# Kernel tuning notes

Hardware: AMD Instinct MI355X
Metric: run time of the kernel (lower is better)

Reference implementation:

```python
import jax, jax.numpy as jnp
import numpy as np

D_MODEL = 1024
NHEAD = 16
HEAD_DIM = D_MODEL // NHEAD  # 64
THETA = 10000.0


def apply_rope(t):
    # t: [B, H, S, D]. Interleaved-pair RoPE (lucidrains rotary-embedding-torch
    # rotate_queries_or_keys), positions = arange(S), theta = 10000.
    B, H, S, D = t.shape
    inv_freq = 1.0 / (THETA ** (jnp.arange(0, D, 2, dtype=jnp.float32) / D))  # [D/2]
    ang = jnp.arange(S, dtype=jnp.float32)[:, None] * inv_freq               # [S, D/2]
    cos = jnp.cos(ang).astype(t.dtype)
    sin = jnp.sin(ang).astype(t.dtype)
    tp = t.reshape(B, H, S, D // 2, 2)
    x1, x2 = tp[..., 0], tp[..., 1]
    rot = jnp.stack([x1 * cos - x2 * sin, x1 * sin + x2 * cos], axis=-1)
    return rot.reshape(B, H, S, D)


def setup_inputs() -> dict:
    key = jax.random.key(0)
    k0, k1, k2, k3, k4 = jax.random.split(key, 5)
    B, Sx, Sc = 2, 2048, 2048
    sc = 0.02  # weight init scale
    return {
        "x": jax.random.normal(k0, (B, Sx, D_MODEL), jnp.float32),
        "context": jax.random.normal(k1, (B, Sc, D_MODEL), jnp.float32),
        "Wq": jax.random.normal(k2, (D_MODEL, D_MODEL), jnp.float32) * sc,
        "Wv": jax.random.normal(k3, (D_MODEL, D_MODEL), jnp.float32) * sc,
        "Wo": jax.random.normal(k4, (D_MODEL, D_MODEL), jnp.float32) * sc,
        "bo": jnp.zeros((D_MODEL,), jnp.float32),
        "x_pos": jnp.arange(B * Sx, dtype=jnp.int64).reshape(B, Sx) % Sx,
        "context_pos": jnp.arange(B * Sc, dtype=jnp.int64).reshape(B, Sc) % Sc,
    }


def reference(x, context, Wq, Wv, Wo, bo, x_pos, context_pos):
    # x_pos/context_pos are unused when both streams use the internal
    # RotaryEmbedding (is_imu1=is_imu2=True), matching the original forward.
    B, Sx, _ = x.shape
    Sc = context.shape[1]
    q = (x @ Wq.T).reshape(B, Sx, NHEAD, HEAD_DIM).transpose(0, 2, 1, 3)
    # NOTE: original code uses projq (not projk) for keys — replicated here.
    k = (context @ Wq.T).reshape(B, Sc, NHEAD, HEAD_DIM).transpose(0, 2, 1, 3)
    v = (context @ Wv.T).reshape(B, Sc, NHEAD, HEAD_DIM).transpose(0, 2, 1, 3)
    q = apply_rope(q)
    k = apply_rope(k)
    scale = 1.0 / jnp.sqrt(jnp.asarray(HEAD_DIM, q.dtype))
    attn = jax.nn.softmax(jnp.einsum("bhqd,bhkd->bhqk", q, k) * scale, axis=-1)
    out = jnp.einsum("bhqk,bhkd->bhqd", attn, v)            # [B,H,Sx,hd]
    out = out.transpose(0, 2, 1, 3).reshape(B, Sx, D_MODEL)  # [B,Sx,d_model]
    return out @ Wo.T + bo
```

## Files before the change

kernel.cpp:

```cpp
#include <hip/hip_runtime.h>
#include <cmath>


typedef __bf16 bf16x8 __attribute__((ext_vector_type(8)));
typedef __bf16 bf16x4 __attribute__((ext_vector_type(4)));
typedef float f32x4 __attribute__((ext_vector_type(4)));

#define MFMA(A, B, C) __builtin_amdgcn_mfma_f32_16x16x32_bf16(A, B, C, 0, 0, 0)
#define GLL16(g, l)                                                        \
  __builtin_amdgcn_global_load_lds(                                        \
      (const __attribute__((address_space(1))) unsigned int*)(g),          \
      (__attribute__((address_space(3))) unsigned int*)(l), 16, 0, 0)

__global__ __launch_bounds__(256) void cvt_all_kernel(
    const float* __restrict__ x, const float* __restrict__ ctx,
    const float* __restrict__ Wq, const float* __restrict__ Wv,
    const float* __restrict__ Wo, __bf16* __restrict__ xb, __bf16* __restrict__ cb,
    __bf16* __restrict__ Wqb, __bf16* __restrict__ Wvb, __bf16* __restrict__ Wob) {
  int base = blockIdx.x * 512 + threadIdx.x;
  const float* src;
  __bf16* dst;
  int off;
  if (base < 1048576) { src = x; dst = xb; off = 0; }
  else if (base < 2097152) { src = ctx; dst = cb; off = 1048576; }
  else if (base < 2359296) { src = Wq; dst = Wqb; off = 2097152; }
  else if (base < 2621440) { src = Wv; dst = Wvb; off = 2359296; }
  else { src = Wo; dst = Wob; off = 2621440; }
#pragma unroll
  for (int jj = 0; jj < 2; jj++) {
    int j = base - off + jj * 256;
    float4 f = ((const float4*)src)[j];
    bf16x4 o;
    o[0] = (__bf16)f.x; o[1] = (__bf16)f.y; o[2] = (__bf16)f.z; o[3] = (__bf16)f.w;
    ((bf16x4*)dst)[j] = o;
  }
}

__global__ __launch_bounds__(256) void gemm_proj(const __bf16* __restrict__ A0,
                                                 const __bf16* __restrict__ W0,
                                                 void* __restrict__ outQ,
                                                 void* __restrict__ outK,
                                                 void* __restrict__ outV) {
  const int tid = threadIdx.x;
  const int wave = tid >> 6, lane = tid & 63, quad = lane >> 4, l15 = lane & 15;
  const int mw = wave >> 1, nw = wave & 1;

  const int id = blockIdx.x;
  int m0, n0;
  const __bf16* A;
  const __bf16* W;
  bool vmode;
  if (id < 512) {
    const int xcd = id & 7, j = id >> 3;
    m0 = (xcd * 8 + (j & 7)) * 128;
    n0 = (j >> 3) * 128;
    A = A0;
    W = W0;
    vmode = false;
  } else {
    const int vid = id - 512;
    const int xcd = vid & 7, j = vid >> 3;
    m0 = (xcd * 4 + (j & 3)) * 128;
    n0 = (j >> 2) * 128;
    A = A0 + (size_t)4096 * 1024;
    W = W0 + (size_t)1024 * 1024;
    vmode = true;
  }

  __shared__ __attribute__((aligned(16))) __bf16 As[3][4096];
  __shared__ __attribute__((aligned(16))) __bf16 Ws[3][4096];

  int goff[2];
#pragma unroll
  for (int jj = 0; jj < 2; jj++) {
    const int s = jj * 256 + tid;
    const int row = s >> 2;
    const int kcg = (s & 3) ^ ((row >> 1) & 3);
    goff[jj] = row * 1024 + kcg * 8;
  }
  const __bf16* Ag = A + (size_t)m0 * 1024;
  const __bf16* Wg = W + (size_t)n0 * 1024;
  const int ldsoff0 = wave * 512;
  const int ldsoff1 = 2048 + wave * 512;

  const int sw = (l15 >> 1) & 3;
  int afoff[4], wfoff[4];
#pragma unroll
  for (int t = 0; t < 4; t++) {
    afoff[t] = (mw * 64 + t * 16 + l15) * 32 + (quad ^ sw) * 8;
    wfoff[t] = (nw * 64 + t * 16 + l15) * 32 + (quad ^ sw) * 8;
  }

  f32x4 acc[4][4] = {};

  auto stage = [&](int buf, int k0) {
    GLL16(Ag + goff[0] + k0, &As[buf][ldsoff0]);
    GLL16(Ag + goff[1] + k0, &As[buf][ldsoff1]);
    GLL16(Wg + goff[0] + k0, &Ws[buf][ldsoff0]);
    GLL16(Wg + goff[1] + k0, &Ws[buf][ldsoff1]);
  };
  auto compute = [&](int buf) {
    bf16x8 af[4], wf[4];
#pragma unroll
    for (int t = 0; t < 4; t++) af[t] = *(const bf16x8*)&As[buf][afoff[t]];
#pragma unroll
    for (int t = 0; t < 4; t++) wf[t] = *(const bf16x8*)&Ws[buf][wfoff[t]];
#pragma unroll
    for (int mt = 0; mt < 4; mt++)
#pragma unroll
      for (int nt = 0; nt < 4; nt++) acc[mt][nt] = MFMA(af[mt], wf[nt], acc[mt][nt]);
  };

  stage(0, 0);
  stage(1, 32);
  int buf = 0;
  for (int c = 0; c < 32; c++) {
    __syncthreads();
    if (c + 2 < 32) {
      int nb = buf + 2;
      if (nb >= 3) nb -= 3;
      stage(nb, (c + 2) * 32);
    }
    compute(buf);
    buf = (buf == 2) ? 0 : buf + 1;
  }

  if (!vmode) {
    const int isK = (m0 >= 4096);
    __bf16* O = (__bf16*)(isK ? outK : outQ);
    const float qsc = isK ? 1.0f : 0.18033688f;
    const int mb = m0 & 4095;
#pragma unroll
    for (int nt = 0; nt < 4; nt++) {
      const int n = n0 + nw * 64 + nt * 16 + l15;
      const int h = n >> 6, d = n & 63, p = d >> 1;
      const float invf_rev =
          __builtin_amdgcn_exp2f(-((float)p * 0.41524101f + 2.6514961f));
#pragma unroll
      for (int mt = 0; mt < 4; mt++) {
#pragma unroll
        for (int r = 0; r < 4; r++) {
          const int row = mb + mw * 64 + mt * 16 + quad * 4 + r;
          const int s = row & 2047, b = row >> 11;
          float v = acc[mt][nt][r];
          float pv = __shfl_xor(v, 1, 64);
          float fr = __builtin_amdgcn_fractf((float)s * invf_rev);
          float sn = __builtin_amdgcn_sinf(fr);
          float cs = __builtin_amdgcn_cosf(fr);
          float res = (lane & 1) ? (pv * sn + v * cs) : (v * cs - pv * sn);
          O[((size_t)(b * 16 + h) * 2048 + s) * 64 + d] = (__bf16)(res * qsc);
        }
      }
    }
  } else {
    __bf16* O = (__bf16*)outV;
#pragma unroll
    for (int nt = 0; nt < 4; nt++) {
      const int n = n0 + nw * 64 + nt * 16 + l15;
      const int h = n >> 6, d = n & 63;
#pragma unroll
      for (int mt = 0; mt < 4; mt++) {
        const int rowb = m0 + mw * 64 + mt * 16 + quad * 4;
        const int s = rowb & 2047, b = rowb >> 11;
        bf16x4 o;
#pragma unroll
        for (int r = 0; r < 4; r++) o[r] = (__bf16)acc[mt][nt][r];
        *(bf16x4*)(O + ((size_t)(b * 16 + h) * 64 + d) * 2048 + s) = o;
      }
    }
  }
}

__global__ __launch_bounds__(256) void gemm_out(const __bf16* __restrict__ A,
                                                const __bf16* __restrict__ W,
                                                float* __restrict__ O,
                                                const float* __restrict__ bias) {
  const int tid = threadIdx.x;
  const int wave = tid >> 6, lane = tid & 63, quad = lane >> 4, l15 = lane & 15;
  const int mw = wave >> 1, nw = wave & 1;
  const int id = blockIdx.x;
  const int xcd = id & 7, j = id >> 3;
  const int m0 = (xcd * 8 + (j & 7)) * 64;
  const int n0 = (j >> 3) * 64;

  __shared__ __attribute__((aligned(16))) __bf16 As[3][2048];
  __shared__ __attribute__((aligned(16))) __bf16 Ws[3][2048];

  const int srow = tid >> 2;
  const int goff = srow * 1024 + (((tid & 3) ^ ((srow >> 1) & 3)) * 8);
  const __bf16* Ag = A + (size_t)m0 * 1024;
  const __bf16* Wg = W + (size_t)n0 * 1024;
  const int ldsoff = wave * 512;

  const int sw = (l15 >> 1) & 3;
  int afoff[2], wfoff[2];
#pragma unroll
  for (int t = 0; t < 2; t++) {
    afoff[t] = (mw * 32 + t * 16 + l15) * 32 + (quad ^ sw) * 8;
    wfoff[t] = (nw * 32 + t * 16 + l15) * 32 + (quad ^ sw) * 8;
  }

  f32x4 acc[2][2] = {};

  auto stage = [&](int buf, int k0) {
    GLL16(Ag + goff + k0, &As[buf][ldsoff]);
    GLL16(Wg + goff + k0, &Ws[buf][ldsoff]);
  };
  auto compute = [&](int buf) {
    bf16x8 af[2], wf[2];
#pragma unroll
    for (int t = 0; t < 2; t++) af[t] = *(const bf16x8*)&As[buf][afoff[t]];
#pragma unroll
    for (int t = 0; t < 2; t++) wf[t] = *(const bf16x8*)&Ws[buf][wfoff[t]];
#pragma unroll
    for (int mt = 0; mt < 2; mt++)
#pragma unroll
      for (int nt = 0; nt < 2; nt++) acc[mt][nt] = MFMA(af[mt], wf[nt], acc[mt][nt]);
  };

  stage(0, 0);
  stage(1, 32);
  int buf = 0;
  for (int c = 0; c < 32; c++) {
    __syncthreads();
    if (c + 2 < 32) {
      int nb = buf + 2;
      if (nb >= 3) nb -= 3;
      stage(nb, (c + 2) * 32);
    }
    compute(buf);
    buf = (buf == 2) ? 0 : buf + 1;
  }

#pragma unroll
  for (int nt = 0; nt < 2; nt++) {
    const int n = n0 + nw * 32 + nt * 16 + l15;
    const float bv = bias[n];
#pragma unroll
    for (int mt = 0; mt < 2; mt++) {
#pragma unroll
      for (int r = 0; r < 4; r++) {
        const int row = m0 + mw * 32 + mt * 16 + quad * 4 + r;
        O[(size_t)row * 1024 + n] = acc[mt][nt][r] + bv;
      }
    }
  }
}

__global__ __launch_bounds__(256) void attn_kernel(const __bf16* __restrict__ Q,
                                                   const __bf16* __restrict__ K,
                                                   const __bf16* __restrict__ Vt,
                                                   __bf16* __restrict__ Aout) {
  const int tid = threadIdx.x;
  const int wave = tid >> 6, lane = tid & 63, quad = lane >> 4, l15 = lane & 15;
  const int id = blockIdx.x;
  const int j = id >> 3;
  const int bh = ((id & 7) << 2) | (j & 3);
  const int q0 = (j >> 2) << 7;

  const __bf16* Qb = Q + (size_t)bh * (2048 * 64);
  const __bf16* Kb = K + (size_t)bh * (2048 * 64);
  const __bf16* Vb = Vt + (size_t)bh * (64 * 2048);

  __shared__ __attribute__((aligned(16))) __bf16 Kbuf[4][4096];
  __shared__ __attribute__((aligned(16))) __bf16 Vbuf[4][4096];
  __shared__ __attribute__((aligned(16))) __bf16 Plds[4][2][8][16][8];

  bf16x8 qf[2][2];
#pragma unroll
  for (int c = 0; c < 2; c++) {
    const __bf16* qp = Qb + (size_t)(q0 + wave * 32 + c * 16 + l15) * 64 + quad * 8;
    qf[c][0] = *(const bf16x8*)qp;
    qf[c][1] = *(const bf16x8*)(qp + 32);
  }

  const int s0 = (wave * 2 + 0) * 64 + lane;
  const int s1 = (wave * 2 + 1) * 64 + lane;
  const int r0 = s0 >> 3, c0 = (s0 & 7) ^ (r0 & 7);
  const int r1 = s1 >> 3, c1 = (s1 & 7) ^ (r1 & 7);
  const __bf16* kg0 = Kb + r0 * 64 + c0 * 8;
  const __bf16* kg1 = Kb + r1 * 64 + c1 * 8;
  const __bf16* vg0 = Vb + r0 * 2048 + c0 * 8;
  const __bf16* vg1 = Vb + r1 * 2048 + c1 * 8;
  const int kldsA = (wave * 2 + 0) * 512;
  const int kldsB = (wave * 2 + 1) * 512;

  const int offF0 = l15 * 64 + ((quad ^ (l15 & 7)) * 8);
  const int offF1 = l15 * 64 + (((4 + quad) ^ (l15 & 7)) * 8);

  f32x4 rs4[2] = {};
  f32x4 oT[4][2] = {};

  auto stage = [&](int buf, int kt) {
    GLL16(kg0 + kt * 64, &Kbuf[buf][kldsA]);
    GLL16(kg1 + kt * 64, &Kbuf[buf][kldsB]);
    GLL16(vg0 + kt, &Vbuf[buf][kldsA]);
    GLL16(vg1 + kt, &Vbuf[buf][kldsB]);
  };
  auto compute = [&](int buf) {
    f32x4 sT[2][4];
#pragma unroll
    for (int nt = 0; nt < 4; nt++) {
      bf16x8 kf0 = *(const bf16x8*)&Kbuf[buf][nt * 1024 + offF0];
      bf16x8 kf1 = *(const bf16x8*)&Kbuf[buf][nt * 1024 + offF1];
#pragma unroll
      for (int c = 0; c < 2; c++) {
        f32x4 z = {};
        z = MFMA(kf0, qf[c][0], z);
        sT[c][nt] = MFMA(kf1, qf[c][1], z);
      }
    }
#pragma unroll
    for (int c = 0; c < 2; c++) {
#pragma unroll
      for (int nt = 0; nt < 4; nt++) {
        bf16x4 pb;
        f32x4 pe;
#pragma unroll
        for (int r = 0; r < 4; r++) {
          pe[r] = __builtin_amdgcn_exp2f(sT[c][nt][r]);
          pb[r] = (__bf16)pe[r];
        }
        rs4[c] += pe;
        const int chunk = nt * 2 + (quad >> 1);
        *(bf16x4*)&Plds[wave][c][chunk][l15 ^ ((chunk & 3) << 1)][(quad & 1) * 4] = pb;
      }
    }
    bf16x8 pf[2][2];
#pragma unroll
    for (int c = 0; c < 2; c++) {
      pf[c][0] = *(const bf16x8*)&Plds[wave][c][quad][l15 ^ (quad << 1)][0];
      pf[c][1] = *(const bf16x8*)&Plds[wave][c][4 + quad][l15 ^ (quad << 1)][0];
    }
#pragma unroll
    for (int nt = 0; nt < 4; nt++) {
      bf16x8 vf0 = *(const bf16x8*)&Vbuf[buf][nt * 1024 + offF0];
      bf16x8 vf1 = *(const bf16x8*)&Vbuf[buf][nt * 1024 + offF1];
#pragma unroll
      for (int c = 0; c < 2; c++) {
        oT[nt][c] = MFMA(vf0, pf[c][0], oT[nt][c]);
        oT[nt][c] = MFMA(vf1, pf[c][1], oT[nt][c]);
      }
    }
  };

  stage(0, 0);
  stage(1, 64);
  for (int kt = 0; kt < 2048; kt += 128) {
    const int p = (kt >> 7) & 1;
    __syncthreads();
    if (kt + 128 < 2048) {
      stage(2 * (p ^ 1), kt + 128);
      stage(2 * (p ^ 1) + 1, kt + 192);
    }
    compute(2 * p);
    compute(2 * p + 1);
  }

  const int b = bh >> 4, h = bh & 15;
#pragma unroll
  for (int c = 0; c < 2; c++) {
    float l = (rs4[c][0] + rs4[c][1]) + (rs4[c][2] + rs4[c][3]);
    l += __shfl_xor(l, 16, 64);
    l += __shfl_xor(l, 32, 64);
    const float inv = 1.f / l;
    const int q = q0 + wave * 32 + c * 16 + l15;
#pragma unroll
    for (int nt = 0; nt < 4; nt++) {
      bf16x4 o;
#pragma unroll
      for (int r = 0; r < 4; r++) o[r] = (__bf16)(oT[nt][c][r] * inv);
      *(bf16x4*)&Aout[((size_t)(b * 2048 + q)) * 1024 + h * 64 + nt * 16 + quad * 4] = o;
    }
  }
}

extern "C" void kernel_launch(void* const* d_in, const int* in_sizes, int n_in,
                              void* d_out, int out_size, void* d_ws, size_t ws_size,
                              hipStream_t stream) {
  const float* x   = (const float*)d_in[0];
  const float* ctx = (const float*)d_in[1];
  const float* Wq  = (const float*)d_in[2];
  const float* Wv  = (const float*)d_in[3];
  const float* Wo  = (const float*)d_in[4];
  const float* bo  = (const float*)d_in[5];

  char* ws = (char*)d_ws;
  const size_t MB = 1024 * 1024;
  __bf16* xb   = (__bf16*)(ws + 0 * MB);
  __bf16* cb   = (__bf16*)(ws + 8 * MB);
  __bf16* Wqb  = (__bf16*)(ws + 16 * MB);
  __bf16* Wvb  = (__bf16*)(ws + 18 * MB);
  __bf16* Wob  = (__bf16*)(ws + 20 * MB);
  __bf16* qh   = (__bf16*)(ws + 22 * MB);
  __bf16* kh   = (__bf16*)(ws + 30 * MB);
  __bf16* vt   = (__bf16*)(ws + 38 * MB);
  __bf16* attn = xb;

  cvt_all_kernel<<<5632, 256, 0, stream>>>(x, ctx, Wq, Wv, Wo, xb, cb, Wqb, Wvb, Wob);

  gemm_proj<<<768, 256, 0, stream>>>(xb, Wqb, (void*)qh, (void*)kh, (void*)vt);

  attn_kernel<<<512, 256, 0, stream>>>(qh, kh, vt, attn);

  gemm_out<<<1024, 256, 0, stream>>>(attn, Wob, (float*)d_out, bo);
}
```

Before: 207.1 us.

## Use 512-thread attention blocks with one 16-query tile per wave; enlarge out-GEMM M tile

The attention kernel moves from 4 waves each handling 32 queries to 8 waves each handling 16 queries. Each wave now stages one K and one V chunk instead of two, and the wave holds fewer registers, which can raise occupancy and latency hiding. In exchange, each K/V fragment read from LDS is reused across fewer queries. Separately, the output GEMM tile grows from 64x64 to 128x64 with four M sub-tiles per wave, halving the grid to 512 blocks and improving reuse of the W operand.

```diff
diff --git a/kernel.cpp b/kernel.cpp
--- a/kernel.cpp
+++ b/kernel.cpp
@@ -180,40 +180,53 @@
   const int mw = wave >> 1, nw = wave & 1;
   const int id = blockIdx.x;
   const int xcd = id & 7, j = id >> 3;
-  const int m0 = (xcd * 8 + (j & 7)) * 64;
-  const int n0 = (j >> 3) * 64;
-
-  __shared__ __attribute__((aligned(16))) __bf16 As[3][2048];
+  const int m0 = (xcd * 4 + (j & 3)) * 128;
+  const int n0 = (j >> 2) * 64;
+
+  __shared__ __attribute__((aligned(16))) __bf16 As[3][4096];
   __shared__ __attribute__((aligned(16))) __bf16 Ws[3][2048];
 
-  const int srow = tid >> 2;
-  const int goff = srow * 1024 + (((tid & 3) ^ ((srow >> 1) & 3)) * 8);
+  int goff[2];
+#pragma unroll
+  for (int jj = 0; jj < 2; jj++) {
+    const int s = jj * 256 + tid;
+    const int row = s >> 2;
+    const int kcg = (s & 3) ^ ((row >> 1) & 3);
+    goff[jj] = row * 1024 + kcg * 8;
+  }
+  const int wrow = tid >> 2;
+  const int wkcg = (tid & 3) ^ ((wrow >> 1) & 3);
+  const int goffw = wrow * 1024 + wkcg * 8;
+
   const __bf16* Ag = A + (size_t)m0 * 1024;
   const __bf16* Wg = W + (size_t)n0 * 1024;
-  const int ldsoff = wave * 512;
+  const int ldsoff0 = wave * 512;
+  const int ldsoff1 = 2048 + wave * 512;
 
   const int sw = (l15 >> 1) & 3;
-  int afoff[2], wfoff[2];
-#pragma unroll
-  for (int t = 0; t < 2; t++) {
-    afoff[t] = (mw * 32 + t * 16 + l15) * 32 + (quad ^ sw) * 8;
+  int afoff[4], wfoff[2];
+#pragma unroll
+  for (int t = 0; t < 4; t++)
+    afoff[t] = (mw * 64 + t * 16 + l15) * 32 + (quad ^ sw) * 8;
+#pragma unroll
+  for (int t = 0; t < 2; t++)
     wfoff[t] = (nw * 32 + t * 16 + l15) * 32 + (quad ^ sw) * 8;
-  }
-
-  f32x4 acc[2][2] = {};
+
+  f32x4 acc[4][2] = {};
 
   auto stage = [&](int buf, int k0) {
-    GLL16(Ag + goff + k0, &As[buf][ldsoff]);
-    GLL16(Wg + goff + k0, &Ws[buf][ldsoff]);
+    GLL16(Ag + goff[0] + k0, &As[buf][ldsoff0]);
+    GLL16(Ag + goff[1] + k0, &As[buf][ldsoff1]);
+    GLL16(Wg + goffw + k0, &Ws[buf][ldsoff0]);
   };
   auto compute = [&](int buf) {
-    bf16x8 af[2], wf[2];
-#pragma unroll
-    for (int t = 0; t < 2; t++) af[t] = *(const bf16x8*)&As[buf][afoff[t]];
+    bf16x8 af[4], wf[2];
+#pragma unroll
+    for (int t = 0; t < 4; t++) af[t] = *(const bf16x8*)&As[buf][afoff[t]];
 #pragma unroll
     for (int t = 0; t < 2; t++) wf[t] = *(const bf16x8*)&Ws[buf][wfoff[t]];
 #pragma unroll
-    for (int mt = 0; mt < 2; mt++)
+    for (int mt = 0; mt < 4; mt++)
 #pragma unroll
       for (int nt = 0; nt < 2; nt++) acc[mt][nt] = MFMA(af[mt], wf[nt], acc[mt][nt]);
   };
@@ -237,17 +250,17 @@
     const int n = n0 + nw * 32 + nt * 16 + l15;
     const float bv = bias[n];
 #pragma unroll
-    for (int mt = 0; mt < 2; mt++) {
+    for (int mt = 0; mt < 4; mt++) {
 #pragma unroll
       for (int r = 0; r < 4; r++) {
-        const int row = m0 + mw * 32 + mt * 16 + quad * 4 + r;
+        const int row = m0 + mw * 64 + mt * 16 + quad * 4 + r;
         O[(size_t)row * 1024 + n] = acc[mt][nt][r] + bv;
       }
     }
   }
 }
 
-__global__ __launch_bounds__(256) void attn_kernel(const __bf16* __restrict__ Q,
+__global__ __launch_bounds__(512) void attn_kernel(const __bf16* __restrict__ Q,
                                                    const __bf16* __restrict__ K,
                                                    const __bf16* __restrict__ Vt,
                                                    __bf16* __restrict__ Aout) {
@@ -264,83 +277,62 @@
 
   __shared__ __attribute__((aligned(16))) __bf16 Kbuf[4][4096];
   __shared__ __attribute__((aligned(16))) __bf16 Vbuf[4][4096];
-  __shared__ __attribute__((aligned(16))) __bf16 Plds[4][2][8][16][8];
-
-  bf16x8 qf[2][2];
-#pragma unroll
-  for (int c = 0; c < 2; c++) {
-    const __bf16* qp = Qb + (size_t)(q0 + wave * 32 + c * 16 + l15) * 64 + quad * 8;
-    qf[c][0] = *(const bf16x8*)qp;
-    qf[c][1] = *(const bf16x8*)(qp + 32);
-  }
-
-  const int s0 = (wave * 2 + 0) * 64 + lane;
-  const int s1 = (wave * 2 + 1) * 64 + lane;
+  __shared__ __attribute__((aligned(16))) __bf16 Plds[8][8][16][8];
+
+  bf16x8 qf[2];
+  {
+    const __bf16* qp = Qb + (size_t)(q0 + wave * 16 + l15) * 64 + quad * 8;
+    qf[0] = *(const bf16x8*)qp;
+    qf[1] = *(const bf16x8*)(qp + 32);
+  }
+
+  const int s0 = wave * 64 + lane;
   const int r0 = s0 >> 3, c0 = (s0 & 7) ^ (r0 & 7);
-  const int r1 = s1 >> 3, c1 = (s1 & 7) ^ (r1 & 7);
   const __bf16* kg0 = Kb + r0 * 64 + c0 * 8;
-  const __bf16* kg1 = Kb + r1 * 64 + c1 * 8;
   const __bf16* vg0 = Vb + r0 * 2048 + c0 * 8;
-  const __bf16* vg1 = Vb + r1 * 2048 + c1 * 8;
-  const int kldsA = (wave * 2 + 0) * 512;
-  const int kldsB = (wave * 2 + 1) * 512;
+  const int klds = wave * 512;
 
   const int offF0 = l15 * 64 + ((quad ^ (l15 & 7)) * 8);
   const int offF1 = l15 * 64 + (((4 + quad) ^ (l15 & 7)) * 8);
 
-  f32x4 rs4[2] = {};
-  f32x4 oT[4][2] = {};
+  f32x4 rs4 = {};
+  f32x4 oT[4] = {};
 
   auto stage = [&](int buf, int kt) {
-    GLL16(kg0 + kt * 64, &Kbuf[buf][kldsA]);
-    GLL16(kg1 + kt * 64, &Kbuf[buf][kldsB]);
-    GLL16(vg0 + kt, &Vbuf[buf][kldsA]);
-    GLL16(vg1 + kt, &Vbuf[buf][kldsB]);
+    GLL16(kg0 + kt * 64, &Kbuf[buf][klds]);
+    GLL16(vg0 + kt, &Vbuf[buf][klds]);
   };
   auto compute = [&](int buf) {
-    f32x4 sT[2][4];
+    f32x4 sT[4];
 #pragma unroll
     for (int nt = 0; nt < 4; nt++) {
       bf16x8 kf0 = *(const bf16x8*)&Kbuf[buf][nt * 1024 + offF0];
       bf16x8 kf1 = *(const bf16x8*)&Kbuf[buf][nt * 1024 + offF1];
-#pragma unroll
-      for (int c = 0; c < 2; c++) {
-        f32x4 z = {};
-        z = MFMA(kf0, qf[c][0], z);
-        sT[c][nt] = MFMA(kf1, qf[c][1], z);
+      f32x4 z = {};
+      z = MFMA(kf0, qf[0], z);
+      sT[nt] = MFMA(kf1, qf[1], z);
+    }
+#pragma unroll
+    for (int nt = 0; nt < 4; nt++) {
+      bf16x4 pb;
+      f32x4 pe;
+#pragma unroll
+      for (int r = 0; r < 4; r++) {
+        pe[r] = __builtin_amdgcn_exp2f(sT[nt][r]);
+        pb[r] = (__bf16)pe[r];
       }
-    }
-#pragma unroll
-    for (int c = 0; c < 2; c++) {
-#pragma unroll
-      for (int nt = 0; nt < 4; nt++) {
-        bf16x4 pb;
-        f32x4 pe;
-#pragma unroll
-        for (int r = 0; r < 4; r++) {
-          pe[r] = __builtin_amdgcn_exp2f(sT[c][nt][r]);
-          pb[r] = (__bf16)pe[r];
-        }
-        rs4[c] += pe;
-        const int chunk = nt * 2 + (quad >> 1);
-        *(bf16x4*)&Plds[wave][c][chunk][l15 ^ ((chunk & 3) << 1)][(quad & 1) * 4] = pb;
-      }
-    }
-    bf16x8 pf[2][2];
-#pragma unroll
-    for (int c = 0; c < 2; c++) {
-      pf[c][0] = *(const bf16x8*)&Plds[wave][c][quad][l15 ^ (quad << 1)][0];
-      pf[c][1] = *(const bf16x8*)&Plds[wave][c][4 + quad][l15 ^ (quad << 1)][0];
-    }
+      rs4 += pe;
+      const int chunk = nt * 2 + (quad >> 1);
+      *(bf16x4*)&Plds[wave][chunk][l15 ^ ((chunk & 3) << 1)][(quad & 1) * 4] = pb;
+    }
+    bf16x8 pf0 = *(const bf16x8*)&Plds[wave][quad][l15 ^ (quad << 1)][0];
+    bf16x8 pf1 = *(const bf16x8*)&Plds[wave][4 + quad][l15 ^ (quad << 1)][0];
 #pragma unroll
     for (int nt = 0; nt < 4; nt++) {
       bf16x8 vf0 = *(const bf16x8*)&Vbuf[buf][nt * 1024 + offF0];
       bf16x8 vf1 = *(const bf16x8*)&Vbuf[buf][nt * 1024 + offF1];
-#pragma unroll
-      for (int c = 0; c < 2; c++) {
-        oT[nt][c] = MFMA(vf0, pf[c][0], oT[nt][c]);
-        oT[nt][c] = MFMA(vf1, pf[c][1], oT[nt][c]);
-      }
+      oT[nt] = MFMA(vf0, pf0, oT[nt]);
+      oT[nt] = MFMA(vf1, pf1, oT[nt]);
     }
   };
 
@@ -358,20 +350,17 @@
   }
 
   const int b = bh >> 4, h = bh & 15;
-#pragma unroll
-  for (int c = 0; c < 2; c++) {
-    float l = (rs4[c][0] + rs4[c][1]) + (rs4[c][2] + rs4[c][3]);
-    l += __shfl_xor(l, 16, 64);
-    l += __shfl_xor(l, 32, 64);
-    const float inv = 1.f / l;
-    const int q = q0 + wave * 32 + c * 16 + l15;
-#pragma unroll
-    for (int nt = 0; nt < 4; nt++) {
-      bf16x4 o;
-#pragma unroll
-      for (int r = 0; r < 4; r++) o[r] = (__bf16)(oT[nt][c][r] * inv);
-      *(bf16x4*)&Aout[((size_t)(b * 2048 + q)) * 1024 + h * 64 + nt * 16 + quad * 4] = o;
-    }
+  float l = (rs4[0] + rs4[1]) + (rs4[2] + rs4[3]);
+  l += __shfl_xor(l, 16, 64);
+  l += __shfl_xor(l, 32, 64);
+  const float inv = 1.f / l;
+  const int q = q0 + wave * 16 + l15;
+#pragma unroll
+  for (int nt = 0; nt < 4; nt++) {
+    bf16x4 o;
+#pragma unroll
+    for (int r = 0; r < 4; r++) o[r] = (__bf16)(oT[nt][r] * inv);
+    *(bf16x4*)&Aout[((size_t)(b * 2048 + q)) * 1024 + h * 64 + nt * 16 + quad * 4] = o;
   }
 }
 
@@ -401,7 +390,7 @@
 
   gemm_proj<<<768, 256, 0, stream>>>(xb, Wqb, (void*)qh, (void*)kh, (void*)vt);
 
-  attn_kernel<<<512, 256, 0, stream>>>(qh, kh, vt, attn);
-
-  gemm_out<<<1024, 256, 0, stream>>>(attn, Wob, (float*)d_out, bo);
-}
+  attn_kernel<<<512, 512, 0, stream>>>(qh, kh, vt, attn);
+
+  gemm_out<<<512, 256, 0, stream>>>(attn, Wob, (float*)d_out, bo);
+}
```

Result: no change. 203.9 us (-1.6%).
